# Kernel optimization log

Measured on AMD Instinct MI355X. Metric: run time of the kernel, lower is better.

## Reference

```python
import jax, jax.numpy as jnp
import numpy as np

K = 512   # per-head dim == input dim
H = 8     # heads

def setup_inputs() -> dict:
    key = jax.random.key(0)
    ks = jax.random.split(key, 6)
    b, t = 4, 2048
    x = jax.random.normal(ks[0], (b, t, K), dtype=jnp.float32)
    s = 0.02
    Wq = jax.random.normal(ks[1], (K, K * H), dtype=jnp.float32) * s
    Wk = jax.random.normal(ks[2], (K, K * H), dtype=jnp.float32) * s
    Wv = jax.random.normal(ks[3], (K, K * H), dtype=jnp.float32) * s
    Wo = jax.random.normal(ks[4], (K * H, K), dtype=jnp.float32) * s
    bo = jnp.zeros((K,), dtype=jnp.float32)
    return {"x": x, "Wq": Wq, "Wk": Wk, "Wv": Wv, "Wo": Wo, "bo": bo}

def reference(x, Wq, Wk, Wv, Wo, bo):
    b, t, _ = x.shape
    scale = K ** 0.25
    # rearrange 'b t (k h) -> (b h) t k' == reshape (b,t,K,H) then move h next to b
    def split_heads(y):
        return y.reshape(b, t, K, H).transpose(0, 3, 1, 2)  # [b,h,t,K]
    q = split_heads(x @ Wq) / scale
    k_ = split_heads(x @ Wk) / scale
    v = split_heads(x @ Wv)
    dot = jnp.einsum('bhtk,bhsk->bhts', q, k_)      # [b,h,t,t]
    attn = jax.nn.softmax(dot, axis=-1)
    o = jnp.einsum('bhts,bhsk->bhtk', attn, v)      # [b,h,t,K]
    # '(b h) t k -> b t (h k)': heads outer in concat
    o = o.transpose(0, 2, 1, 3).reshape(b, t, H * K)
    return o @ Wo + bo
```

## Files before the change

kernel.cpp:

```cpp
#include <hip/hip_runtime.h>

typedef unsigned short u16;
typedef unsigned char u8;
typedef unsigned int u32;
typedef long i64;
typedef __attribute__((ext_vector_type(8))) short bf16x8;
typedef __attribute__((ext_vector_type(4))) float f32x4;
typedef __attribute__((ext_vector_type(4))) u16 u16x4;

__device__ __forceinline__ u16 f2bf(float f) {
  u32 u = __builtin_bit_cast(u32, f);
  return (u16)((u + 0x7FFFu + ((u >> 16) & 1u)) >> 16);
}
__device__ __forceinline__ u8 f2fp8(float f) {
  int w = __builtin_amdgcn_cvt_pk_fp8_f32(f, 0.f, 0, false);
  return (u8)(w & 0xff);
}

__device__ __forceinline__ f32x4 mfma16(bf16x8 a, bf16x8 b, f32x4 c) {
  return __builtin_amdgcn_mfma_f32_16x16x32_bf16(a, b, c, 0, 0, 0);
}
__device__ __forceinline__ f32x4 mfma16f8(i64 a, i64 b, f32x4 c) {
  return __builtin_amdgcn_mfma_f32_16x16x32_fp8_fp8(a, b, c, 0, 0, 0);
}

__device__ __forceinline__ void gload16(const void* g, void* l) {
  __builtin_amdgcn_global_load_lds(
      (const __attribute__((address_space(1))) unsigned int*)g,
      (__attribute__((address_space(3))) unsigned int*)l, 16, 0, 0);
}

__device__ __forceinline__ u32 cvtpk(float lo, float hi) {
  u32 r;
  asm volatile("v_cvt_pk_bf16_f32 %0, %1, %2" : "=v"(r) : "v"(lo), "v"(hi));
  return r;
}


__global__ void pack_x_kernel(const float* __restrict__ x, u16* __restrict__ xb) {
  const int i = blockIdx.x * 256 + threadIdx.x;
  const float4 v = ((const float4*)x)[i];
  u16x4 o;
  o[0] = f2bf(v.x); o[1] = f2bf(v.y); o[2] = f2bf(v.z); o[3] = f2bf(v.w);
  ((u16x4*)xb)[i] = o;
}

__global__ void pack_wqkv_t(const float* __restrict__ W, u16* __restrict__ Wp) {
  __shared__ u16 tile[64][72];
  const int t = threadIdx.x;
  const int c0 = blockIdx.x * 64, dd0 = blockIdx.y * 64;
#pragma unroll
  for (int s = 0; s < 4; ++s) {
    const int r = s * 16 + (t >> 4);
    const int q = (t & 15) * 4;
    const float4 v = *(const float4*)&W[(size_t)(dd0 + r) * 4096 + c0 + q];
    tile[r][q + 0] = f2bf(v.x); tile[r][q + 1] = f2bf(v.y);
    tile[r][q + 2] = f2bf(v.z); tile[r][q + 3] = f2bf(v.w);
  }
  __syncthreads();
#pragma unroll
  for (int s = 0; s < 4; ++s) {
    const int cl = s * 16 + (t >> 4);
    const int u = t & 15;
    const int cg = c0 + cl;
    const int orow = (cg & 7) * 512 + (cg >> 3);
    u16x4 o;
#pragma unroll
    for (int i = 0; i < 4; ++i) o[i] = tile[u * 4 + i][cl];
    *(u16x4*)&Wp[(size_t)orow * 512 + dd0 + u * 4] = o;
  }
}

__global__ void pack_wo_t(const float* __restrict__ W, u16* __restrict__ Wp) {
  __shared__ u16 tile[64][72];
  const int t = threadIdx.x;
  const int k0 = blockIdx.x * 64, n0 = blockIdx.y * 64;
#pragma unroll
  for (int s = 0; s < 4; ++s) {
    const int r = s * 16 + (t >> 4);
    const int q = (t & 15) * 4;
    const float4 v = *(const float4*)&W[(size_t)(k0 + r) * 512 + n0 + q];
    tile[r][q + 0] = f2bf(v.x); tile[r][q + 1] = f2bf(v.y);
    tile[r][q + 2] = f2bf(v.z); tile[r][q + 3] = f2bf(v.w);
  }
  __syncthreads();
#pragma unroll
  for (int s = 0; s < 4; ++s) {
    const int cl = s * 16 + (t >> 4);
    const int u = t & 15;
    u16x4 o;
#pragma unroll
    for (int i = 0; i < 4; ++i) o[i] = tile[u * 4 + i][cl];
    *(u16x4*)&Wp[(size_t)(n0 + cl) * 4096 + k0 + u * 4] = o;
  }
}


template <int MODE>
__global__ __launch_bounds__(256, 2) void gemm_bf16(
    const u16* __restrict__ A, const u16* __restrict__ B,
    void* __restrict__ Cout, const float* __restrict__ bias,
    int Kd, float scale) {
  __shared__ u16 Al[128 * 64];
  __shared__ u16 Bl[128 * 64];
  const int tid = threadIdx.x;
  const int lane = tid & 63;
  const int w = tid >> 6, wm = w >> 1, wn = w & 1;
  const int l15 = lane & 15, lg = lane >> 4;
  const int m0 = blockIdx.y * 128, n0 = blockIdx.x * 128;

  f32x4 acc[4][4];
  const f32x4 zero = {0.f, 0.f, 0.f, 0.f};
#pragma unroll
  for (int i = 0; i < 4; ++i)
#pragma unroll
    for (int j = 0; j < 4; ++j) acc[i][j] = zero;

  const int nk = Kd >> 6;
  for (int kt = 0; kt < nk; ++kt) {
    __syncthreads();
    const int k0 = kt << 6;
#pragma unroll
    for (int s = 0; s < 4; ++s) {
      const int chunk = s * 256 + tid;
      const int row = chunk >> 3, c = chunk & 7;
      const int cs = c ^ (row & 7);
      gload16(A + (size_t)(m0 + row) * Kd + k0 + cs * 8, &Al[chunk * 8]);
    }
#pragma unroll
    for (int s = 0; s < 4; ++s) {
      const int chunk = s * 256 + tid;
      const int row = chunk >> 3, c = chunk & 7;
      const int cs = c ^ (row & 7);
      gload16(B + (size_t)(n0 + row) * Kd + k0 + cs * 8, &Bl[chunk * 8]);
    }
    __syncthreads();
#pragma unroll
    for (int kk = 0; kk < 2; ++kk) {
      bf16x8 af[4], bfr[4];
      const int ch = kk * 4 + lg;
#pragma unroll
      for (int i = 0; i < 4; ++i) {
        const int ar = wm * 64 + i * 16 + l15;
        af[i] = *(const bf16x8*)&Al[ar * 64 + ((ch ^ (ar & 7)) * 8)];
        const int br = wn * 64 + i * 16 + l15;
        bfr[i] = *(const bf16x8*)&Bl[br * 64 + ((ch ^ (br & 7)) * 8)];
      }
#pragma unroll
      for (int i = 0; i < 4; ++i)
#pragma unroll
        for (int j = 0; j < 4; ++j)
          acc[i][j] = mfma16(af[i], bfr[j], acc[i][j]);
    }
  }

#pragma unroll
  for (int i = 0; i < 4; ++i) {
    const int gr0 = m0 + wm * 64 + i * 16 + lg * 4;
#pragma unroll
    for (int j = 0; j < 4; ++j) {
      const int gc = n0 + wn * 64 + j * 16 + l15;
      if constexpr (MODE == 0) {
        u8* O = (u8*)Cout;
        const int h = gc >> 9, d = gc & 511;
#pragma unroll
        for (int r = 0; r < 4; ++r) {
          const int grr = gr0 + r;
          const int bb = grr >> 11, t = grr & 2047;
          O[((size_t)((bb * 8 + h) * 2048 + t) << 9) + d] = f2fp8(acc[i][j][r] * scale);
        }
      } else if constexpr (MODE == 1) {
        u16* O = (u16*)Cout;
        const int h = gc >> 9, d = gc & 511;
        const int bb = gr0 >> 11, t = gr0 & 2047;
        u16x4 pk;
#pragma unroll
        for (int r = 0; r < 4; ++r) pk[r] = f2bf(acc[i][j][r]);
        *(u16x4*)&O[((size_t)((bb * 8 + h) * 512 + d) << 11) + t] = pk;
      } else {
        float* O = (float*)Cout;
        const float bv = bias[gc];
#pragma unroll
        for (int r = 0; r < 4; ++r)
          O[(size_t)(gr0 + r) * 512 + gc] = acc[i][j][r] + bv;
      }
    }
  }
}


__global__ __launch_bounds__(512, 2) void attn_kernel(
    const u8* __restrict__ Qg, const u8* __restrict__ Kg,
    const u16* __restrict__ Vtg, u16* __restrict__ Og, int nbh_pxcd) {
  __shared__ u8 K8[2][32 * 512];
  __shared__ u16 Vt_lds[2][512 * 32];
  __shared__ u16 P_lds[4][2][16][32];
  __shared__ float Lsum[8][2][16];

  const int tid = threadIdx.x;
  const int lane = tid & 63;
  const int w = tid >> 6;
  const int pr = w >> 1, whalf = w & 1;
  const int l15 = lane & 15, lg = lane >> 4;

  const int bid = blockIdx.x;
  const int x8 = bid & 7, rest = bid >> 3;
  const int qt = rest & 15;
  const int bh = x8 * nbh_pxcd + (rest >> 4);

  const u8* Qb = Qg + (size_t)bh * 2048 * 512;
  const u8* Kb = Kg + (size_t)bh * 2048 * 512;
  const u16* Vb = Vtg + (size_t)bh * 2048 * 512;

  i64 qf8[2][16];
#pragma unroll
  for (int qtile = 0; qtile < 2; ++qtile) {
    const int qrow = qt * 128 + pr * 32 + qtile * 16 + l15;
    const u8* qp = Qb + (size_t)qrow * 512 + lg * 8;
#pragma unroll
    for (int cc = 0; cc < 16; ++cc) qf8[qtile][cc] = *(const i64*)(qp + cc * 32);
  }

  f32x4 acc[2][16];
#pragma unroll
  for (int i = 0; i < 2; ++i)
#pragma unroll
    for (int j = 0; j < 16; ++j) acc[i][j] = {};
  float lsum0 = 0.f, lsum1 = 0.f;

  const int krow = whalf * 16 + l15;
  const int kswz = (krow & 15) << 1;

#define STAGE_K8(tile, buf)                                                   \
  {                                                                           \
    _Pragma("unroll") for (int s_ = 0; s_ < 2; ++s_) {                        \
      const int ch = s_ * 512 + tid;                                          \
      const int row = ch >> 5, p_ = ch & 31;                                  \
      const int ps = p_ ^ ((row & 15) << 1);                                  \
      gload16(Kb + (size_t)((tile) * 32 + row) * 512 + ps * 16,               \
              &K8[buf][ch * 16]);                                             \
    }                                                                         \
  }
#define STAGE_V(tile, buf)                                                    \
  {                                                                           \
    _Pragma("unroll") for (int s_ = 0; s_ < 4; ++s_) {                        \
      const int chunk = s_ * 512 + tid;                                       \
      const int row = chunk >> 2, c_ = chunk & 3;                             \
      const int cs = c_ ^ ((row >> 1) & 3);                                   \
      gload16(Vb + (size_t)row * 2048 + (tile) * 32 + cs * 8,                 \
              &Vt_lds[buf][chunk * 8]);                                       \
    }                                                                         \
  }

  STAGE_K8(0, 0);
  STAGE_V(0, 0);
  asm volatile("s_waitcnt vmcnt(0)" ::: "memory");
  __builtin_amdgcn_s_barrier();

  for (int t = 0; t < 64; ++t) {
    const int cur = t & 1;

    if (t < 63) {
      STAGE_K8(t + 1, cur ^ 1);
      STAGE_V(t + 1, cur ^ 1);
    }

    f32x4 s0a = {}, s0b = {}, s1a = {}, s1b = {};
    {
      const u8* kbase = &K8[cur][krow * 512 + (lg & 1) * 8];
      const int phalf = lg >> 1;
#pragma unroll
      for (int cc = 0; cc < 8; ++cc) {
        const int p = (cc * 2 + phalf) ^ kswz;
        i64 kf = *(const i64*)(kbase + p * 16);
        s0a = mfma16f8(kf, qf8[0][cc], s0a);
        s1a = mfma16f8(kf, qf8[1][cc], s1a);
      }
#pragma unroll
      for (int cc = 8; cc < 16; ++cc) {
        const int p = (cc * 2 + phalf) ^ kswz;
        i64 kf = *(const i64*)(kbase + p * 16);
        s0b = mfma16f8(kf, qf8[0][cc], s0b);
        s1b = mfma16f8(kf, qf8[1][cc], s1b);
      }
    }
    f32x4 s0, s1;
#pragma unroll
    for (int r = 0; r < 4; ++r) {
      s0[r] = s0a[r] + s0b[r];
      s1[r] = s1a[r] + s1b[r];
    }

#pragma unroll
    for (int r = 0; r < 4; ++r) {
      s0[r] = __expf(s0[r]);
      lsum0 += s0[r];
      s1[r] = __expf(s1[r]);
      lsum1 += s1[r];
    }

    {
      const int kvbase = whalf * 16 + lg * 4;
      u16x4 pk0, pk1;
      u32 a0 = cvtpk(s0[0], s0[1]), a1 = cvtpk(s0[2], s0[3]);
      u32 b0 = cvtpk(s1[0], s1[1]), b1 = cvtpk(s1[2], s1[3]);
      pk0 = __builtin_bit_cast(u16x4, ((unsigned long long)a1 << 32) | a0);
      pk1 = __builtin_bit_cast(u16x4, ((unsigned long long)b1 << 32) | b0);
      *(u16x4*)&P_lds[pr][0][l15][kvbase] = pk0;
      *(u16x4*)&P_lds[pr][1][l15][kvbase] = pk1;
    }
    asm volatile("s_waitcnt lgkmcnt(0)" ::: "memory");
    __builtin_amdgcn_s_barrier();

    {
      bf16x8 pfr[2];
      pfr[0] = *(const bf16x8*)&P_lds[pr][0][l15][lg * 8];
      pfr[1] = *(const bf16x8*)&P_lds[pr][1][l15][lg * 8];
#pragma unroll
      for (int dtile = 0; dtile < 16; ++dtile) {
        const int drow = whalf * 256 + dtile * 16 + l15;
        const int pos = lg ^ ((drow >> 1) & 3);
        bf16x8 vf = *(const bf16x8*)&Vt_lds[cur][drow * 32 + pos * 8];
        acc[0][dtile] = mfma16(vf, pfr[0], acc[0][dtile]);
        acc[1][dtile] = mfma16(vf, pfr[1], acc[1][dtile]);
      }
    }

    asm volatile("s_waitcnt vmcnt(0) lgkmcnt(0)" ::: "memory");
    __builtin_amdgcn_s_barrier();
  }

  lsum0 += __shfl_xor(lsum0, 16, 64);
  lsum0 += __shfl_xor(lsum0, 32, 64);
  lsum1 += __shfl_xor(lsum1, 16, 64);
  lsum1 += __shfl_xor(lsum1, 32, 64);
  if (lane < 16) {
    Lsum[w][0][l15] = lsum0;
    Lsum[w][1][l15] = lsum1;
  }
  __syncthreads();
  const float inv0 = 1.0f / (Lsum[w][0][l15] + Lsum[w ^ 1][0][l15]);
  const float inv1 = 1.0f / (Lsum[w][1][l15] + Lsum[w ^ 1][1][l15]);

  const int bb = bh >> 3, h = bh & 7;
#pragma unroll
  for (int qtile = 0; qtile < 2; ++qtile) {
    const float inv = qtile ? inv1 : inv0;
    const int q = qt * 128 + pr * 32 + qtile * 16 + l15;
    u16* orow_p = Og + (size_t)(bb * 2048 + q) * 4096 + h * 512 + whalf * 256;
#pragma unroll
    for (int dtile = 0; dtile < 16; ++dtile) {
      u16x4 pk;
#pragma unroll
      for (int r = 0; r < 4; ++r) pk[r] = f2bf(acc[qtile][dtile][r] * inv);
      *(u16x4*)(orow_p + dtile * 16 + lg * 4) = pk;
    }
  }
#undef STAGE_K8
#undef STAGE_V
}


extern "C" void kernel_launch(void* const* d_in, const int* in_sizes, int n_in,
                              void* d_out, int out_size, void* d_ws, size_t ws_size,
                              hipStream_t stream) {
  const float* x = (const float*)d_in[0];
  const float* Wq = (const float*)d_in[1];
  const float* Wk = (const float*)d_in[2];
  const float* Wv = (const float*)d_in[3];
  const float* Wo = (const float*)d_in[4];
  const float* bo = (const float*)d_in[5];
  float* out = (float*)d_out;

  const size_t MB = 1ull << 20;
  int BB;
  if (ws_size >= 216 * MB) BB = 4;
  else if (ws_size >= 120 * MB) BB = 2;
  else BB = 1;

  char* ws = (char*)d_ws;
  u16* xb  = (u16*)(ws);
  u16* Wqp = (u16*)(ws + 8 * MB);
  u16* Wkp = (u16*)(ws + 12 * MB);
  u16* Wvp = (u16*)(ws + 16 * MB);
  u16* Wot = (u16*)(ws + 20 * MB);
  u8*  Qg  = (u8*)(ws + 24 * MB);
  u8*  Kg  = (u8*)(ws + (24 + 8 * (size_t)BB) * MB);
  u16* Vtg = (u16*)(ws + (24 + 16 * (size_t)BB) * MB);
  u16* Og  = (u16*)(ws + (24 + 32 * (size_t)BB) * MB);

  pack_x_kernel<<<dim3(4096), dim3(256), 0, stream>>>(x, xb);
  pack_wqkv_t<<<dim3(64, 8), dim3(256), 0, stream>>>(Wq, Wqp);
  pack_wqkv_t<<<dim3(64, 8), dim3(256), 0, stream>>>(Wk, Wkp);
  pack_wqkv_t<<<dim3(64, 8), dim3(256), 0, stream>>>(Wv, Wvp);
  pack_wo_t<<<dim3(64, 8), dim3(256), 0, stream>>>(Wo, Wot);

  const float qk_scale = 0.21022410381342865f;

  const int nchunk = 4 / BB;
  for (int c = 0; c < nchunk; ++c) {
    const u16* Ax = xb + (size_t)c * BB * 2048 * 512;
    gemm_bf16<0><<<dim3(32, BB * 16), dim3(256), 0, stream>>>(Ax, Wqp, (void*)Qg, nullptr, 512, qk_scale);
    gemm_bf16<0><<<dim3(32, BB * 16), dim3(256), 0, stream>>>(Ax, Wkp, (void*)Kg, nullptr, 512, qk_scale);
    gemm_bf16<1><<<dim3(32, BB * 16), dim3(256), 0, stream>>>(Ax, Wvp, (void*)Vtg, nullptr, 512, 1.0f);

    attn_kernel<<<dim3(16 * BB * 8), dim3(512), 0, stream>>>(Qg, Kg, Vtg, Og, BB);

    gemm_bf16<2><<<dim3(4, BB * 16), dim3(256), 0, stream>>>(
        Og, Wot, (void*)(out + (size_t)c * BB * 2048 * 512), bo, 4096, 1.0f);
  }
}
```

Before: 531.6 us.

## Software-pipeline PV matmul one tile behind QK and narrow output GEMM tile

The attention loop now writes P into a double-buffered LDS slot and runs the P·V MFMAs for the previous tile after computing scores for the current one. This removes the mid-iteration barrier between the P write and the P·V read. V staging moves to a triple buffer so the lagged tile is still resident, which raises LDS use. Separately, the output projection GEMM gets a BN template parameter and runs with 64-wide N tiles. That doubles its grid from 4 to 8 column blocks to give more parallelism across CUs.

Result: no change. 524.0 us (-1.4%).

```diff
diff --git a/kernel.cpp b/kernel.cpp
--- a/kernel.cpp
+++ b/kernel.cpp
@@ -96,25 +96,25 @@
 }
 
 
-template <int MODE>
+template <int MODE, int BN>
 __global__ __launch_bounds__(256, 2) void gemm_bf16(
     const u16* __restrict__ A, const u16* __restrict__ B,
     void* __restrict__ Cout, const float* __restrict__ bias,
     int Kd, float scale) {
+  constexpr int JT = BN / 32;
   __shared__ u16 Al[128 * 64];
-  __shared__ u16 Bl[128 * 64];
+  __shared__ u16 Bl[BN * 64];
   const int tid = threadIdx.x;
   const int lane = tid & 63;
   const int w = tid >> 6, wm = w >> 1, wn = w & 1;
   const int l15 = lane & 15, lg = lane >> 4;
-  const int m0 = blockIdx.y * 128, n0 = blockIdx.x * 128;
-
-  f32x4 acc[4][4];
-  const f32x4 zero = {0.f, 0.f, 0.f, 0.f};
+  const int m0 = blockIdx.y * 128, n0 = blockIdx.x * BN;
+
+  f32x4 acc[4][JT];
 #pragma unroll
   for (int i = 0; i < 4; ++i)
 #pragma unroll
-    for (int j = 0; j < 4; ++j) acc[i][j] = zero;
+    for (int j = 0; j < JT; ++j) acc[i][j] = {};
 
   const int nk = Kd >> 6;
   for (int kt = 0; kt < nk; ++kt) {
@@ -128,7 +128,7 @@
       gload16(A + (size_t)(m0 + row) * Kd + k0 + cs * 8, &Al[chunk * 8]);
     }
 #pragma unroll
-    for (int s = 0; s < 4; ++s) {
+    for (int s = 0; s < BN / 32; ++s) {
       const int chunk = s * 256 + tid;
       const int row = chunk >> 3, c = chunk & 7;
       const int cs = c ^ (row & 7);
@@ -137,19 +137,22 @@
     __syncthreads();
 #pragma unroll
     for (int kk = 0; kk < 2; ++kk) {
-      bf16x8 af[4], bfr[4];
+      bf16x8 af[4], bfr[JT];
       const int ch = kk * 4 + lg;
 #pragma unroll
       for (int i = 0; i < 4; ++i) {
         const int ar = wm * 64 + i * 16 + l15;
         af[i] = *(const bf16x8*)&Al[ar * 64 + ((ch ^ (ar & 7)) * 8)];
-        const int br = wn * 64 + i * 16 + l15;
-        bfr[i] = *(const bf16x8*)&Bl[br * 64 + ((ch ^ (br & 7)) * 8)];
       }
 #pragma unroll
+      for (int j = 0; j < JT; ++j) {
+        const int br = wn * (BN / 2) + j * 16 + l15;
+        bfr[j] = *(const bf16x8*)&Bl[br * 64 + ((ch ^ (br & 7)) * 8)];
+      }
+#pragma unroll
       for (int i = 0; i < 4; ++i)
 #pragma unroll
-        for (int j = 0; j < 4; ++j)
+        for (int j = 0; j < JT; ++j)
           acc[i][j] = mfma16(af[i], bfr[j], acc[i][j]);
     }
   }
@@ -158,8 +161,8 @@
   for (int i = 0; i < 4; ++i) {
     const int gr0 = m0 + wm * 64 + i * 16 + lg * 4;
 #pragma unroll
-    for (int j = 0; j < 4; ++j) {
-      const int gc = n0 + wn * 64 + j * 16 + l15;
+    for (int j = 0; j < JT; ++j) {
+      const int gc = n0 + wn * (BN / 2) + j * 16 + l15;
       if constexpr (MODE == 0) {
         u8* O = (u8*)Cout;
         const int h = gc >> 9, d = gc & 511;
@@ -193,8 +196,8 @@
     const u8* __restrict__ Qg, const u8* __restrict__ Kg,
     const u16* __restrict__ Vtg, u16* __restrict__ Og, int nbh_pxcd) {
   __shared__ u8 K8[2][32 * 512];
-  __shared__ u16 Vt_lds[2][512 * 32];
-  __shared__ u16 P_lds[4][2][16][32];
+  __shared__ u16 V3[3][512 * 32];
+  __shared__ u16 P_lds[2][4][2][16][32];
   __shared__ float Lsum[8][2][16];
 
   const int tid = threadIdx.x;
@@ -248,7 +251,20 @@
       const int row = chunk >> 2, c_ = chunk & 3;                             \
       const int cs = c_ ^ ((row >> 1) & 3);                                   \
       gload16(Vb + (size_t)row * 2048 + (tile) * 32 + cs * 8,                 \
-              &Vt_lds[buf][chunk * 8]);                                       \
+              &V3[buf][chunk * 8]);                                           \
+    }                                                                         \
+  }
+
+#define PV_LAG(par, vbuf)                                                     \
+  {                                                                           \
+    bf16x8 pfr0 = *(const bf16x8*)&P_lds[par][pr][0][l15][lg * 8];            \
+    bf16x8 pfr1 = *(const bf16x8*)&P_lds[par][pr][1][l15][lg * 8];            \
+    _Pragma("unroll") for (int dtile = 0; dtile < 16; ++dtile) {              \
+      const int drow = whalf * 256 + dtile * 16 + l15;                        \
+      const int pos = lg ^ ((drow >> 1) & 3);                                 \
+      bf16x8 vf = *(const bf16x8*)&V3[vbuf][drow * 32 + pos * 8];             \
+      acc[0][dtile] = mfma16(vf, pfr0, acc[0][dtile]);                        \
+      acc[1][dtile] = mfma16(vf, pfr1, acc[1][dtile]);                        \
     }                                                                         \
   }
 
@@ -257,12 +273,15 @@
   asm volatile("s_waitcnt vmcnt(0)" ::: "memory");
   __builtin_amdgcn_s_barrier();
 
+  int vstage = 1;
+  int vread = 2;
+
   for (int t = 0; t < 64; ++t) {
     const int cur = t & 1;
 
     if (t < 63) {
       STAGE_K8(t + 1, cur ^ 1);
-      STAGE_V(t + 1, cur ^ 1);
+      STAGE_V(t + 1, vstage);
     }
 
     f32x4 s0a = {}, s0b = {}, s1a = {}, s1b = {};
@@ -287,48 +306,32 @@
     f32x4 s0, s1;
 #pragma unroll
     for (int r = 0; r < 4; ++r) {
-      s0[r] = s0a[r] + s0b[r];
-      s1[r] = s1a[r] + s1b[r];
-    }
-
-#pragma unroll
-    for (int r = 0; r < 4; ++r) {
-      s0[r] = __expf(s0[r]);
+      s0[r] = __expf(s0a[r] + s0b[r]);
       lsum0 += s0[r];
-      s1[r] = __expf(s1[r]);
+      s1[r] = __expf(s1a[r] + s1b[r]);
       lsum1 += s1[r];
     }
 
     {
       const int kvbase = whalf * 16 + lg * 4;
-      u16x4 pk0, pk1;
       u32 a0 = cvtpk(s0[0], s0[1]), a1 = cvtpk(s0[2], s0[3]);
       u32 b0 = cvtpk(s1[0], s1[1]), b1 = cvtpk(s1[2], s1[3]);
-      pk0 = __builtin_bit_cast(u16x4, ((unsigned long long)a1 << 32) | a0);
-      pk1 = __builtin_bit_cast(u16x4, ((unsigned long long)b1 << 32) | b0);
-      *(u16x4*)&P_lds[pr][0][l15][kvbase] = pk0;
-      *(u16x4*)&P_lds[pr][1][l15][kvbase] = pk1;
-    }
-    asm volatile("s_waitcnt lgkmcnt(0)" ::: "memory");
-    __builtin_amdgcn_s_barrier();
-
-    {
-      bf16x8 pfr[2];
-      pfr[0] = *(const bf16x8*)&P_lds[pr][0][l15][lg * 8];
-      pfr[1] = *(const bf16x8*)&P_lds[pr][1][l15][lg * 8];
-#pragma unroll
-      for (int dtile = 0; dtile < 16; ++dtile) {
-        const int drow = whalf * 256 + dtile * 16 + l15;
-        const int pos = lg ^ ((drow >> 1) & 3);
-        bf16x8 vf = *(const bf16x8*)&Vt_lds[cur][drow * 32 + pos * 8];
-        acc[0][dtile] = mfma16(vf, pfr[0], acc[0][dtile]);
-        acc[1][dtile] = mfma16(vf, pfr[1], acc[1][dtile]);
-      }
-    }
+      u16x4 pk0 = __builtin_bit_cast(u16x4, ((unsigned long long)a1 << 32) | a0);
+      u16x4 pk1 = __builtin_bit_cast(u16x4, ((unsigned long long)b1 << 32) | b0);
+      *(u16x4*)&P_lds[cur][pr][0][l15][kvbase] = pk0;
+      *(u16x4*)&P_lds[cur][pr][1][l15][kvbase] = pk1;
+    }
+
+    if (t > 0) PV_LAG(cur ^ 1, vread);
 
     asm volatile("s_waitcnt vmcnt(0) lgkmcnt(0)" ::: "memory");
     __builtin_amdgcn_s_barrier();
-  }
+
+    vstage = (vstage == 2) ? 0 : vstage + 1;
+    vread = (vread == 2) ? 0 : vread + 1;
+  }
+
+  PV_LAG(1, vread);
 
   lsum0 += __shfl_xor(lsum0, 16, 64);
   lsum0 += __shfl_xor(lsum0, 32, 64);
@@ -358,6 +361,7 @@
   }
 #undef STAGE_K8
 #undef STAGE_V
+#undef PV_LAG
 }
 
 
@@ -400,13 +404,13 @@
   const int nchunk = 4 / BB;
   for (int c = 0; c < nchunk; ++c) {
     const u16* Ax = xb + (size_t)c * BB * 2048 * 512;
-    gemm_bf16<0><<<dim3(32, BB * 16), dim3(256), 0, stream>>>(Ax, Wqp, (void*)Qg, nullptr, 512, qk_scale);
-    gemm_bf16<0><<<dim3(32, BB * 16), dim3(256), 0, stream>>>(Ax, Wkp, (void*)Kg, nullptr, 512, qk_scale);
-    gemm_bf16<1><<<dim3(32, BB * 16), dim3(256), 0, stream>>>(Ax, Wvp, (void*)Vtg, nullptr, 512, 1.0f);
+    gemm_bf16<0, 128><<<dim3(32, BB * 16), dim3(256), 0, stream>>>(Ax, Wqp, (void*)Qg, nullptr, 512, qk_scale);
+    gemm_bf16<0, 128><<<dim3(32, BB * 16), dim3(256), 0, stream>>>(Ax, Wkp, (void*)Kg, nullptr, 512, qk_scale);
+    gemm_bf16<1, 128><<<dim3(32, BB * 16), dim3(256), 0, stream>>>(Ax, Wvp, (void*)Vtg, nullptr, 512, 1.0f);
 
     attn_kernel<<<dim3(16 * BB * 8), dim3(512), 0, stream>>>(Qg, Kg, Vtg, Og, BB);
 
-    gemm_bf16<2><<<dim3(4, BB * 16), dim3(256), 0, stream>>>(
+    gemm_bf16<2, 64><<<dim3(8, BB * 16), dim3(256), 0, stream>>>(
         Og, Wot, (void*)(out + (size_t)c * BB * 2048 * 512), bo, 4096, 1.0f);
   }
 }
```
